# Performance work log

Measured on AMD Instinct MI355X. Metric: run time of the kernel, lower is better.

Reference implementation:

```python
import jax, jax.numpy as jnp
import numpy as np

INPUT_SIZE = 512
HIDDEN_SIZE = 512
BATCH = 64
SEQ = 1024

def _xavier(key, shape):
    fan_in, fan_out = shape
    limit = float(np.sqrt(6.0 / (fan_in + fan_out)))
    return jax.random.uniform(key, shape, jnp.float32, -limit, limit)

def setup_inputs() -> dict:
    key = jax.random.key(0)
    ks = jax.random.split(key, 9)
    x = jax.random.normal(ks[0], (BATCH, SEQ, INPUT_SIZE), jnp.float32)
    # Concatenate the 4 input-hidden and 4 hidden-hidden weights (i,f,g,o order)
    W_i = jnp.concatenate([_xavier(ks[1 + j], (INPUT_SIZE, HIDDEN_SIZE)) for j in range(4)], axis=1)  # [I, 4H]
    W_h = jnp.concatenate([_xavier(ks[5 + j], (HIDDEN_SIZE, HIDDEN_SIZE)) for j in range(4)], axis=1)  # [H, 4H]
    b = jnp.zeros((4 * HIDDEN_SIZE,), jnp.float32)  # b_ii+b_hi etc. are both zero-init; combined bias
    return {"x": x, "W_i": W_i, "W_h": W_h, "b": b}

def reference(x, W_i, W_h, b):
    H = W_h.shape[0]
    B = x.shape[0]
    # Precompute all input projections in one big GEMM: [B, S, 4H]
    x_proj = jnp.einsum('bsi,ig->bsg', x, W_i) + b

    def step(carry, xp_t):
        h, c = carry
        gates = xp_t + h @ W_h  # [B, 4H]
        i_t = jax.nn.sigmoid(gates[:, 0*H:1*H])
        f_t = jax.nn.sigmoid(gates[:, 1*H:2*H])
        g_t = jnp.tanh(gates[:, 2*H:3*H])
        o_t = jax.nn.sigmoid(gates[:, 3*H:4*H])
        c = f_t * c + i_t * g_t
        h = o_t * jnp.tanh(c)
        return (h, c), None

    h0 = jnp.zeros((B, H), x.dtype)
    c0 = jnp.zeros((B, H), x.dtype)
    (h_t, c_t), _ = jax.lax.scan(step, (h0, c0), jnp.swapaxes(x_proj, 0, 1))
    return (h_t, c_t)
```

## Files before the change

kernel.cpp:

```cpp
#include <hip/hip_runtime.h>
#include <hip/hip_bf16.h>
#include <hip/hip_cooperative_groups.h>

namespace cg = cooperative_groups;

typedef unsigned short ushort_t;
typedef unsigned int uint32;
typedef __attribute__((ext_vector_type(8))) __bf16 bf16x8;
typedef __attribute__((ext_vector_type(4))) float f32x4;
typedef __attribute__((ext_vector_type(4))) unsigned int u32x4;

#define SEQ_LEN 1024
#define NWG 32
#define NTHR 256

#define XPACK_BYTES (64ull << 20)
#define WPACK_BYTES (4ull << 20)
#define HB_OFF  (XPACK_BYTES + WPACK_BYTES)
#define FLG_OFF (HB_OFF + (128ull << 10))
#define WS_NEED (FLG_OFF + (4ull << 10))

__device__ __forceinline__ ushort_t f2bf(float f) {
  unsigned u = __builtin_bit_cast(unsigned, f);
  unsigned r = (u + 0x7fffu + ((u >> 16) & 1u)) >> 16;
  return (ushort_t)r;
}
__device__ __forceinline__ float sigm(float x) {
  float e = __expf(-x);
  return __builtin_amdgcn_rcpf(1.f + e);
}
__device__ __forceinline__ float tanh_fast(float x) {
  float a = fabsf(x);
  float e = __expf(-2.f * a);
  float r = (1.f - e) * __builtin_amdgcn_rcpf(1.f + e);
  return copysignf(r, x);
}

__global__ void zero_mem_kernel(u32x4* p) {
  int i = blockIdx.x * blockDim.x + threadIdx.x;
  u32x4 z = {0u, 0u, 0u, 0u};
  p[i] = z;
}

__global__ void pack_x_kernel(const float* __restrict__ x, u32x4* __restrict__ xp) {
  unsigned u = blockIdx.x * blockDim.x + threadIdx.x;
  int lane = u & 63;
  int kk   = (u >> 6) & 15;
  int bq   = (u >> 10) & 3;
  int t    = u >> 12;
  int hi2 = lane >> 4, lo = lane & 15;
  int b  = bq * 16 + lo;
  int k0 = kk * 32 + hi2 * 8;
  const float* src = x + ((size_t)b * SEQ_LEN + t) * 512 + k0;
  f32x4 f0 = *(const f32x4*)(src);
  f32x4 f1 = *(const f32x4*)(src + 4);
  u32x4 o;
  o[0] = f2bf(f0[0]) | ((uint32)f2bf(f0[1]) << 16);
  o[1] = f2bf(f0[2]) | ((uint32)f2bf(f0[3]) << 16);
  o[2] = f2bf(f1[0]) | ((uint32)f2bf(f1[1]) << 16);
  o[3] = f2bf(f1[2]) | ((uint32)f2bf(f1[3]) << 16);
  xp[u] = o;
}

__global__ void pack_w_kernel(const float* __restrict__ Wi, const float* __restrict__ Wh,
                              ushort_t* __restrict__ wp) {
  unsigned e = blockIdx.x * blockDim.x + threadIdx.x;
  int k = e >> 11;
  int col = e & 2047;
  float v = (k < 512) ? Wi[(size_t)k * 2048 + col] : Wh[(size_t)(k - 512) * 2048 + col];
  int wg  = (col & 511) >> 4;
  int tau = (col >> 2) & 3;
  int hcl = col & 3;
  int gate = col >> 9;
  int p = (hcl << 2) | gate;
  int kk = k >> 5;
  int hi = (k >> 3) & 3;
  int r = k & 7;
  int lane = (hi << 4) | p;
  wp[(size_t)wg * 65536 + (size_t)((kk * 4 + tau) * 64 + lane) * 8 + r] = f2bf(v);
}

template<bool FAST>
__global__ void __launch_bounds__(NTHR, 1)
lstm_coop(const float* __restrict__ x, const float* __restrict__ Wi,
          const float* __restrict__ Wh, const float* __restrict__ bias,
          const u32x4* __restrict__ xpack, const u32x4* __restrict__ wpack,
          ushort_t* hbuf, uint32* flags, float* out)
{
  __shared__ u32x4 lA[8192];
  const int tid  = threadIdx.x;
  const int wg   = blockIdx.x;
  const int lane = tid & 63;
  const int wv   = tid >> 6;
  const int hi2  = lane >> 4;
  const int lo   = lane & 15;
  const int b    = (wv << 4) | lo;

  if constexpr (FAST) {
    const u32x4* wsrc = wpack + (size_t)wg * 8192;
    for (int i = tid; i < 8192; i += NTHR) lA[i] = wsrc[i];
  } else {
    for (int uu = tid; uu < 8192; uu += NTHR) {
      int ln = uu & 63, tau = (uu >> 6) & 3, kk = uu >> 8;
      int uhi = ln >> 4, p = ln & 15;
      int gate = p & 3, hcl = p >> 2;
      int col = gate * 512 + (wg << 4) + tau * 4 + hcl;
      ushort_t tmp[8];
#pragma unroll
      for (int r = 0; r < 8; ++r) {
        int k = (kk << 5) + (uhi << 3) + r;
        float f = (k < 512) ? Wi[(size_t)k * 2048 + col] : Wh[(size_t)(k - 512) * 2048 + col];
        tmp[r] = f2bf(f);
      }
      u32x4 v;
      v[0] = tmp[0] | ((uint32)tmp[1] << 16);
      v[1] = tmp[2] | ((uint32)tmp[3] << 16);
      v[2] = tmp[4] | ((uint32)tmp[5] << 16);
      v[3] = tmp[6] | ((uint32)tmp[7] << 16);
      lA[uu] = v;
    }
  }
  __syncthreads();

  int kh[4], uoff[4];
  float bia[4][4];
#pragma unroll
  for (int tau = 0; tau < 4; ++tau) {
    int k = (wg << 4) + tau * 4 + hi2;
    kh[tau] = k;
    uoff[tau] = ((wv * 1024 + (k >> 5) * 64 + ((k >> 3) & 3) * 16 + lo) << 3) + (k & 7);
#pragma unroll
    for (int g = 0; g < 4; ++g) bia[tau][g] = bias[g * 512 + k];
  }

  float c[4] = {0.f, 0.f, 0.f, 0.f};
  float hn[4] = {0.f, 0.f, 0.f, 0.f};

  for (int t = 0; t < SEQ_LEN; ++t) {
    f32x4 ax0 = {bia[0][0], bia[0][1], bia[0][2], bia[0][3]};
    f32x4 ax1 = {bia[1][0], bia[1][1], bia[1][2], bia[1][3]};
    f32x4 ax2 = {bia[2][0], bia[2][1], bia[2][2], bia[2][3]};
    f32x4 ax3 = {bia[3][0], bia[3][1], bia[3][2], bia[3][3]};
#pragma unroll
    for (int kk = 0; kk < 16; ++kk) {
      bf16x8 xv;
      if constexpr (FAST) {
        xv = __builtin_bit_cast(bf16x8, xpack[(size_t)t * 4096 + wv * 1024 + kk * 64 + lane]);
      } else {
        const float* xr = x + ((size_t)b * SEQ_LEN + t) * 512 + (kk << 5) + (hi2 << 3);
        f32x4 f0 = *(const f32x4*)(xr);
        f32x4 f1 = *(const f32x4*)(xr + 4);
        u32x4 v;
        v[0] = f2bf(f0[0]) | ((uint32)f2bf(f0[1]) << 16);
        v[1] = f2bf(f0[2]) | ((uint32)f2bf(f0[3]) << 16);
        v[2] = f2bf(f1[0]) | ((uint32)f2bf(f1[1]) << 16);
        v[3] = f2bf(f1[2]) | ((uint32)f2bf(f1[3]) << 16);
        xv = __builtin_bit_cast(bf16x8, v);
      }
      ax0 = __builtin_amdgcn_mfma_f32_16x16x32_bf16(
              __builtin_bit_cast(bf16x8, lA[(kk * 4 + 0) * 64 + lane]), xv, ax0, 0, 0, 0);
      ax1 = __builtin_amdgcn_mfma_f32_16x16x32_bf16(
              __builtin_bit_cast(bf16x8, lA[(kk * 4 + 1) * 64 + lane]), xv, ax1, 0, 0, 0);
      ax2 = __builtin_amdgcn_mfma_f32_16x16x32_bf16(
              __builtin_bit_cast(bf16x8, lA[(kk * 4 + 2) * 64 + lane]), xv, ax2, 0, 0, 0);
      ax3 = __builtin_amdgcn_mfma_f32_16x16x32_bf16(
              __builtin_bit_cast(bf16x8, lA[(kk * 4 + 3) * 64 + lane]), xv, ax3, 0, 0, 0);
    }

    if (t > 0) {
      if constexpr (FAST) {
        const uint32* fa = flags + wv * 32 + (lane & 31);
        const uint32 tt = (uint32)t;
        while (true) {
          uint32 v;
          asm volatile("global_load_dword %0, %1, off sc0 sc1\n\ts_waitcnt vmcnt(0)"
                       : "=v"(v) : "v"(fa) : "memory");
          if (__all(v >= tt)) break;
        }
        __builtin_amdgcn_sched_barrier(0);
      }
      const u32x4* hr = (const u32x4*)(hbuf + (size_t)(t & 1) * 32768) + wv * 1024 + lane;
      u32x4 hreg[16];
      if constexpr (FAST) {
#pragma unroll
        for (int kk = 0; kk < 16; ++kk)
          asm volatile("global_load_dwordx4 %0, %1, off sc0 sc1"
                       : "=v"(hreg[kk]) : "v"(hr + kk * 64) : "memory");
        asm volatile("s_waitcnt vmcnt(0)" ::: "memory");
        __builtin_amdgcn_sched_barrier(0);
      } else {
#pragma unroll
        for (int kk = 0; kk < 16; ++kk) hreg[kk] = hr[kk * 64];
      }
#pragma unroll
      for (int kk = 0; kk < 16; ++kk) {
        bf16x8 hv = __builtin_bit_cast(bf16x8, hreg[kk]);
        ax0 = __builtin_amdgcn_mfma_f32_16x16x32_bf16(
                __builtin_bit_cast(bf16x8, lA[((16 + kk) * 4 + 0) * 64 + lane]), hv, ax0, 0, 0, 0);
        ax1 = __builtin_amdgcn_mfma_f32_16x16x32_bf16(
                __builtin_bit_cast(bf16x8, lA[((16 + kk) * 4 + 1) * 64 + lane]), hv, ax1, 0, 0, 0);
        ax2 = __builtin_amdgcn_mfma_f32_16x16x32_bf16(
                __builtin_bit_cast(bf16x8, lA[((16 + kk) * 4 + 2) * 64 + lane]), hv, ax2, 0, 0, 0);
        ax3 = __builtin_amdgcn_mfma_f32_16x16x32_bf16(
                __builtin_bit_cast(bf16x8, lA[((16 + kk) * 4 + 3) * 64 + lane]), hv, ax3, 0, 0, 0);
      }
    }

    f32x4 axv[4] = {ax0, ax1, ax2, ax3};
#pragma unroll
    for (int tau = 0; tau < 4; ++tau) {
      float gi = axv[tau][0], gf = axv[tau][1], gg = axv[tau][2], go = axv[tau][3];
      float it = sigm(gi), ft = sigm(gf), ot = sigm(go), gt = tanh_fast(gg);
      c[tau] = ft * c[tau] + it * gt;
      hn[tau] = ot * tanh_fast(c[tau]);
    }

    if (t < SEQ_LEN - 1) {
      ushort_t* hw = hbuf + (size_t)((t + 1) & 1) * 32768;
      if constexpr (FAST) {
#pragma unroll
        for (int tau = 0; tau < 4; ++tau) {
          uint32 v = f2bf(hn[tau]);
          asm volatile("global_store_short %0, %1, off sc0 sc1"
                       :: "v"(hw + uoff[tau]), "v"(v) : "memory");
        }
        asm volatile("s_waitcnt vmcnt(0)" ::: "memory");
        __builtin_amdgcn_sched_barrier(0);
        if (lane == 0) {
          uint32* fp = flags + wv * 32 + wg;
          uint32 val = (uint32)(t + 1);
          asm volatile("global_store_dword %0, %1, off sc0 sc1"
                       :: "v"(fp), "v"(val) : "memory");
        }
      } else {
#pragma unroll
        for (int tau = 0; tau < 4; ++tau) hw[uoff[tau]] = f2bf(hn[tau]);
        __threadfence();
        cg::this_grid().sync();
        __threadfence();
      }
    } else {
      if constexpr (!FAST) {
        __threadfence();
        cg::this_grid().sync();
      }
    }
  }

#pragma unroll
  for (int tau = 0; tau < 4; ++tau) {
    out[(size_t)b * 512 + kh[tau]] = hn[tau];
    out[32768 + (size_t)b * 512 + kh[tau]] = c[tau];
  }
}

extern "C" void kernel_launch(void* const* d_in, const int* in_sizes, int n_in,
                              void* d_out, int out_size, void* d_ws, size_t ws_size,
                              hipStream_t stream) {
  const float* x    = (const float*)d_in[0];
  const float* Wi   = (const float*)d_in[1];
  const float* Wh   = (const float*)d_in[2];
  const float* bias = (const float*)d_in[3];
  float* out = (float*)d_out;

  bool fast = (d_ws != nullptr) && (ws_size >= WS_NEED);

  if (fast) {
    const u32x4* xpack = (const u32x4*)d_ws;
    const u32x4* wpack = (const u32x4*)((char*)d_ws + XPACK_BYTES);
    ushort_t* hbuf = (ushort_t*)((char*)d_ws + HB_OFF);
    uint32* flags  = (uint32*)((char*)d_ws + FLG_OFF);

    zero_mem_kernel<<<1, 32, 0, stream>>>((u32x4*)((char*)d_ws + FLG_OFF));
    pack_x_kernel<<<16384, 256, 0, stream>>>(x, (u32x4*)d_ws);
    pack_w_kernel<<<8192, 256, 0, stream>>>(Wi, Wh, (ushort_t*)((char*)d_ws + XPACK_BYTES));

    lstm_coop<true><<<dim3(NWG), dim3(NTHR), 0, stream>>>(
        x, Wi, Wh, bias, xpack, wpack, hbuf, flags, out);
  } else {
    ushort_t* hbuf = (ushort_t*)d_out;
    uint32* flags = (uint32*)d_out;
    const u32x4* xpack = (const u32x4*)x;
    const u32x4* wpack = (const u32x4*)Wi;

    void* args[] = {(void*)&x, (void*)&Wi, (void*)&Wh, (void*)&bias,
                    (void*)&xpack, (void*)&wpack, (void*)&hbuf, (void*)&flags, (void*)&out};
    void (*kfn)(const float*, const float*, const float*, const float*,
                const u32x4*, const u32x4*, ushort_t*, uint32*, float*) = lstm_coop<false>;
    hipLaunchCooperativeKernel(reinterpret_cast<void*>(kfn), dim3(NWG), dim3(NTHR),
                               args, 0, stream);
  }
}
```

Measured before the change: 3.883 ms.

## Split LSTM into producer/consumer workgroups with ring-buffered input projections

Replaces the single persistent kernel with 64 workgroups of 512 threads. 32 producer workgroups compute the input projection x·W_i plus bias up to 16 timesteps ahead and write it into a flag-guarded ring buffer in the workspace. 32 consumer workgroups keep W_h in registers and run only the recurrent h·W_h matmul and gate math on the serial critical path. This removes the separate x-packing pass and takes the input GEMM off the per-step dependency chain. The cost is more flag polling, extra global traffic through the ring, and a reliance on all 64 workgroups being resident at once.

```diff
diff --git a/kernel.cpp b/kernel.cpp
--- a/kernel.cpp
+++ b/kernel.cpp
@@ -11,14 +11,14 @@
 typedef __attribute__((ext_vector_type(4))) unsigned int u32x4;
 
 #define SEQ_LEN 1024
-#define NWG 32
-#define NTHR 256
-
-#define XPACK_BYTES (64ull << 20)
-#define WPACK_BYTES (4ull << 20)
-#define HB_OFF  (XPACK_BYTES + WPACK_BYTES)
-#define FLG_OFF (HB_OFF + (128ull << 10))
-#define WS_NEED (FLG_OFF + (4ull << 10))
+#define RSLOT 16
+
+#define WPACK_OFF 0ull
+#define RING_OFF  (4ull << 20)
+#define HX_OFF    (RING_OFF + (8ull << 20))
+#define HFLG_OFF  (HX_OFF + (128ull << 10))
+#define XFLG_OFF  (HFLG_OFF + (1ull << 10))
+#define WS_NEED   (XFLG_OFF + (1ull << 10))
 
 __device__ __forceinline__ ushort_t f2bf(float f) {
   unsigned u = __builtin_bit_cast(unsigned, f);
@@ -35,31 +35,12 @@
   float r = (1.f - e) * __builtin_amdgcn_rcpf(1.f + e);
   return copysignf(r, x);
 }
+__device__ __forceinline__ uint32 umin2(uint32 a, uint32 b) { return a < b ? a : b; }
 
 __global__ void zero_mem_kernel(u32x4* p) {
   int i = blockIdx.x * blockDim.x + threadIdx.x;
   u32x4 z = {0u, 0u, 0u, 0u};
   p[i] = z;
-}
-
-__global__ void pack_x_kernel(const float* __restrict__ x, u32x4* __restrict__ xp) {
-  unsigned u = blockIdx.x * blockDim.x + threadIdx.x;
-  int lane = u & 63;
-  int kk   = (u >> 6) & 15;
-  int bq   = (u >> 10) & 3;
-  int t    = u >> 12;
-  int hi2 = lane >> 4, lo = lane & 15;
-  int b  = bq * 16 + lo;
-  int k0 = kk * 32 + hi2 * 8;
-  const float* src = x + ((size_t)b * SEQ_LEN + t) * 512 + k0;
-  f32x4 f0 = *(const f32x4*)(src);
-  f32x4 f1 = *(const f32x4*)(src + 4);
-  u32x4 o;
-  o[0] = f2bf(f0[0]) | ((uint32)f2bf(f0[1]) << 16);
-  o[1] = f2bf(f0[2]) | ((uint32)f2bf(f0[3]) << 16);
-  o[2] = f2bf(f1[0]) | ((uint32)f2bf(f1[1]) << 16);
-  o[3] = f2bf(f1[2]) | ((uint32)f2bf(f1[3]) << 16);
-  xp[u] = o;
 }
 
 __global__ void pack_w_kernel(const float* __restrict__ Wi, const float* __restrict__ Wh,
@@ -68,24 +49,227 @@
   int k = e >> 11;
   int col = e & 2047;
   float v = (k < 512) ? Wi[(size_t)k * 2048 + col] : Wh[(size_t)(k - 512) * 2048 + col];
-  int wg  = (col & 511) >> 4;
-  int tau = (col >> 2) & 3;
-  int hcl = col & 3;
+  int tile = (col & 511) >> 2;
+  int hcl  = col & 3;
   int gate = col >> 9;
   int p = (hcl << 2) | gate;
-  int kk = k >> 5;
+  int part = k >> 9;
+  int kk = (k >> 5) & 15;
   int hi = (k >> 3) & 3;
   int r = k & 7;
   int lane = (hi << 4) | p;
-  wp[(size_t)wg * 65536 + (size_t)((kk * 4 + tau) * 64 + lane) * 8 + r] = f2bf(v);
-}
-
-template<bool FAST>
-__global__ void __launch_bounds__(NTHR, 1)
-lstm_coop(const float* __restrict__ x, const float* __restrict__ Wi,
+  wp[(size_t)((tile * 32 + part * 16 + kk) * 64 + lane) * 8 + r] = f2bf(v);
+}
+
+__global__ __launch_bounds__(512, 1) void lstm_fast(
+    const float* __restrict__ x, const float* __restrict__ bias,
+    const u32x4* __restrict__ wpack, uint32* __restrict__ ring,
+    ushort_t* __restrict__ hx, uint32* __restrict__ hflg,
+    uint32* __restrict__ xflg, float* __restrict__ out)
+{
+  const int tid  = threadIdx.x;
+  const int lane = tid & 63;
+  const int wv   = tid >> 6;
+  const int bq   = wv & 3;
+  const int th   = wv >> 2;
+  const int hi2  = lane >> 4;
+  const int lo   = lane & 15;
+  const int b    = bq * 16 + lo;
+
+  const bool consumer = (blockIdx.x < 32);
+  const int wgr   = consumer ? blockIdx.x : (blockIdx.x - 32);
+  const int pair  = wgr * 2 + th;
+  const int tileA = pair * 2, tileB = pair * 2 + 1;
+  const int pid   = wgr * 8 + wv;
+  const int khA   = pair * 8 + hi2;
+  const int khB   = khA + 4;
+
+  if (consumer) {
+    bf16x8 wA[16], wB[16];
+    {
+      const u32x4* wa = wpack + ((size_t)tileA * 32 + 16) * 64 + lane;
+      const u32x4* wb = wpack + ((size_t)tileB * 32 + 16) * 64 + lane;
+#pragma unroll
+      for (int kk = 0; kk < 16; ++kk) {
+        wA[kk] = __builtin_bit_cast(bf16x8, wa[kk * 64]);
+        wB[kk] = __builtin_bit_cast(bf16x8, wb[kk * 64]);
+      }
+    }
+    const int hoffA = ((bq * 16 + (khA >> 5)) * 64 + ((khA >> 3) & 3) * 16 + lo) * 8 + (khA & 7);
+    const int hoffB = ((bq * 16 + (khB >> 5)) * 64 + ((khB >> 3) & 3) * 16 + lo) * 8 + (khB & 7);
+
+    float cA = 0.f, cB = 0.f, hA = 0.f, hB = 0.f;
+
+    for (int t = 0; t < SEQ_LEN; ++t) {
+      {
+        const uint32* xfp = xflg + pid;
+        const u32x4* hfp = (const u32x4*)hflg + lane;
+        const uint32 need_x = (uint32)(t + 1);
+        const uint32 need_h = (uint32)t;
+        while (true) {
+          uint32 xf; u32x4 hf;
+          asm volatile("global_load_dword %0, %2, off sc0 sc1\n\t"
+                       "global_load_dwordx4 %1, %3, off sc0 sc1\n\t"
+                       "s_waitcnt vmcnt(0)"
+                       : "=&v"(xf), "=&v"(hf) : "v"(xfp), "v"(hfp) : "memory");
+          __builtin_amdgcn_sched_barrier(0);
+          uint32 mn = umin2(umin2(hf[0], hf[1]), umin2(hf[2], hf[3]));
+          bool ok = (xf >= need_x) && (t == 0 || mn >= need_h);
+          if (__all(ok)) break;
+        }
+      }
+      u32x4 xpAu, xpBu;
+      {
+        const u32x4* rbase = (const u32x4*)ring + ((size_t)(t & (RSLOT - 1)) * 128) * 256;
+        const u32x4* rpA = rbase + ((size_t)tileA * 4 + bq) * 64 + lane;
+        const u32x4* rpB = rbase + ((size_t)tileB * 4 + bq) * 64 + lane;
+        asm volatile("global_load_dwordx4 %0, %1, off sc0 sc1"
+                     : "=v"(xpAu) : "v"(rpA) : "memory");
+        asm volatile("global_load_dwordx4 %0, %1, off sc0 sc1"
+                     : "=v"(xpBu) : "v"(rpB) : "memory");
+      }
+      f32x4 gA, gB;
+      if (t == 0) {
+        asm volatile("s_waitcnt vmcnt(0)" ::: "memory");
+        __builtin_amdgcn_sched_barrier(0);
+        gA = __builtin_bit_cast(f32x4, xpAu);
+        gB = __builtin_bit_cast(f32x4, xpBu);
+      } else {
+        u32x4 hreg[16];
+        const u32x4* hr = (const u32x4*)(hx + (size_t)(t & 1) * 32768) + bq * 1024 + lane;
+#pragma unroll
+        for (int kk = 0; kk < 16; ++kk)
+          asm volatile("global_load_dwordx4 %0, %1, off sc0 sc1"
+                       : "=v"(hreg[kk]) : "v"(hr + kk * 64) : "memory");
+        asm volatile("s_waitcnt vmcnt(0)" ::: "memory");
+        __builtin_amdgcn_sched_barrier(0);
+        f32x4 aA0 = __builtin_bit_cast(f32x4, xpAu);
+        f32x4 aB0 = __builtin_bit_cast(f32x4, xpBu);
+        f32x4 aA1 = {0.f, 0.f, 0.f, 0.f};
+        f32x4 aB1 = {0.f, 0.f, 0.f, 0.f};
+#pragma unroll
+        for (int kk = 0; kk < 16; kk += 2) {
+          bf16x8 h0 = __builtin_bit_cast(bf16x8, hreg[kk]);
+          bf16x8 h1 = __builtin_bit_cast(bf16x8, hreg[kk + 1]);
+          aA0 = __builtin_amdgcn_mfma_f32_16x16x32_bf16(wA[kk], h0, aA0, 0, 0, 0);
+          aB0 = __builtin_amdgcn_mfma_f32_16x16x32_bf16(wB[kk], h0, aB0, 0, 0, 0);
+          aA1 = __builtin_amdgcn_mfma_f32_16x16x32_bf16(wA[kk + 1], h1, aA1, 0, 0, 0);
+          aB1 = __builtin_amdgcn_mfma_f32_16x16x32_bf16(wB[kk + 1], h1, aB1, 0, 0, 0);
+        }
+        gA = aA0 + aA1;
+        gB = aB0 + aB1;
+      }
+      {
+        float it = sigm(gA[0]), ft = sigm(gA[1]), ot = sigm(gA[3]), gt = tanh_fast(gA[2]);
+        cA = ft * cA + it * gt;
+        hA = ot * tanh_fast(cA);
+      }
+      {
+        float it = sigm(gB[0]), ft = sigm(gB[1]), ot = sigm(gB[3]), gt = tanh_fast(gB[2]);
+        cB = ft * cB + it * gt;
+        hB = ot * tanh_fast(cB);
+      }
+      if (t < SEQ_LEN - 1) {
+        ushort_t* hw = hx + (size_t)((t + 1) & 1) * 32768;
+        uint32 vA = f2bf(hA), vB = f2bf(hB);
+        asm volatile("global_store_short %0, %1, off sc0 sc1"
+                     :: "v"(hw + hoffA), "v"(vA) : "memory");
+        asm volatile("global_store_short %0, %1, off sc0 sc1"
+                     :: "v"(hw + hoffB), "v"(vB) : "memory");
+        asm volatile("s_waitcnt vmcnt(0)" ::: "memory");
+        __builtin_amdgcn_sched_barrier(0);
+        if (lane == 0) {
+          uint32* fp = hflg + pid;
+          uint32 val = (uint32)(t + 1);
+          asm volatile("global_store_dword %0, %1, off sc0 sc1"
+                       :: "v"(fp), "v"(val) : "memory");
+        }
+      }
+    }
+    out[(size_t)b * 512 + khA] = hA;
+    out[(size_t)b * 512 + khB] = hB;
+    out[32768 + (size_t)b * 512 + khA] = cA;
+    out[32768 + (size_t)b * 512 + khB] = cB;
+  } else {
+    bf16x8 wA[16], wB[16];
+    {
+      const u32x4* wa = wpack + ((size_t)tileA * 32) * 64 + lane;
+      const u32x4* wb = wpack + ((size_t)tileB * 32) * 64 + lane;
+#pragma unroll
+      for (int kk = 0; kk < 16; ++kk) {
+        wA[kk] = __builtin_bit_cast(bf16x8, wa[kk * 64]);
+        wB[kk] = __builtin_bit_cast(bf16x8, wb[kk * 64]);
+      }
+    }
+    f32x4 biaA = {bias[0 * 512 + khA], bias[1 * 512 + khA],
+                  bias[2 * 512 + khA], bias[3 * 512 + khA]};
+    f32x4 biaB = {bias[0 * 512 + khB], bias[1 * 512 + khB],
+                  bias[2 * 512 + khB], bias[3 * 512 + khB]};
+
+    for (int t = 0; t < SEQ_LEN; ++t) {
+      bf16x8 xv[16];
+      {
+        const float* xr = x + ((size_t)b * SEQ_LEN + t) * 512 + (hi2 << 3);
+#pragma unroll
+        for (int kk = 0; kk < 16; ++kk) {
+          f32x4 f0 = *(const f32x4*)(xr + (kk << 5));
+          f32x4 f1 = *(const f32x4*)(xr + (kk << 5) + 4);
+          u32x4 v;
+          v[0] = f2bf(f0[0]) | ((uint32)f2bf(f0[1]) << 16);
+          v[1] = f2bf(f0[2]) | ((uint32)f2bf(f0[3]) << 16);
+          v[2] = f2bf(f1[0]) | ((uint32)f2bf(f1[1]) << 16);
+          v[3] = f2bf(f1[2]) | ((uint32)f2bf(f1[3]) << 16);
+          xv[kk] = __builtin_bit_cast(bf16x8, v);
+        }
+      }
+      if (t >= RSLOT) {
+        const uint32* gp = hflg + pid;
+        const uint32 need = (uint32)(t - RSLOT + 1);
+        while (true) {
+          uint32 v;
+          asm volatile("global_load_dword %0, %1, off sc0 sc1\n\ts_waitcnt vmcnt(0)"
+                       : "=v"(v) : "v"(gp) : "memory");
+          if (__all(v >= need)) break;
+        }
+        __builtin_amdgcn_sched_barrier(0);
+      }
+      f32x4 aA0 = biaA, aB0 = biaB;
+      f32x4 aA1 = {0.f, 0.f, 0.f, 0.f};
+      f32x4 aB1 = {0.f, 0.f, 0.f, 0.f};
+#pragma unroll
+      for (int kk = 0; kk < 16; kk += 2) {
+        aA0 = __builtin_amdgcn_mfma_f32_16x16x32_bf16(wA[kk], xv[kk], aA0, 0, 0, 0);
+        aB0 = __builtin_amdgcn_mfma_f32_16x16x32_bf16(wB[kk], xv[kk], aB0, 0, 0, 0);
+        aA1 = __builtin_amdgcn_mfma_f32_16x16x32_bf16(wA[kk + 1], xv[kk + 1], aA1, 0, 0, 0);
+        aB1 = __builtin_amdgcn_mfma_f32_16x16x32_bf16(wB[kk + 1], xv[kk + 1], aB1, 0, 0, 0);
+      }
+      u32x4 rA = __builtin_bit_cast(u32x4, aA0 + aA1);
+      u32x4 rB = __builtin_bit_cast(u32x4, aB0 + aB1);
+      {
+        u32x4* rbase = (u32x4*)ring + ((size_t)(t & (RSLOT - 1)) * 128) * 256;
+        u32x4* rpA = rbase + ((size_t)tileA * 4 + bq) * 64 + lane;
+        u32x4* rpB = rbase + ((size_t)tileB * 4 + bq) * 64 + lane;
+        asm volatile("global_store_dwordx4 %0, %1, off sc0 sc1"
+                     :: "v"(rpA), "v"(rA) : "memory");
+        asm volatile("global_store_dwordx4 %0, %1, off sc0 sc1"
+                     :: "v"(rpB), "v"(rB) : "memory");
+        asm volatile("s_waitcnt vmcnt(0)" ::: "memory");
+        __builtin_amdgcn_sched_barrier(0);
+        if (lane == 0) {
+          uint32* fp = xflg + pid;
+          uint32 val = (uint32)(t + 1);
+          asm volatile("global_store_dword %0, %1, off sc0 sc1"
+                       :: "v"(fp), "v"(val) : "memory");
+        }
+      }
+    }
+  }
+}
+
+__global__ void __launch_bounds__(256, 1)
+lstm_slow(const float* __restrict__ x, const float* __restrict__ Wi,
           const float* __restrict__ Wh, const float* __restrict__ bias,
-          const u32x4* __restrict__ xpack, const u32x4* __restrict__ wpack,
-          ushort_t* hbuf, uint32* flags, float* out)
+          ushort_t* hbuf, float* out)
 {
   __shared__ u32x4 lA[8192];
   const int tid  = threadIdx.x;
@@ -96,29 +280,24 @@
   const int lo   = lane & 15;
   const int b    = (wv << 4) | lo;
 
-  if constexpr (FAST) {
-    const u32x4* wsrc = wpack + (size_t)wg * 8192;
-    for (int i = tid; i < 8192; i += NTHR) lA[i] = wsrc[i];
-  } else {
-    for (int uu = tid; uu < 8192; uu += NTHR) {
-      int ln = uu & 63, tau = (uu >> 6) & 3, kk = uu >> 8;
-      int uhi = ln >> 4, p = ln & 15;
-      int gate = p & 3, hcl = p >> 2;
-      int col = gate * 512 + (wg << 4) + tau * 4 + hcl;
-      ushort_t tmp[8];
-#pragma unroll
-      for (int r = 0; r < 8; ++r) {
-        int k = (kk << 5) + (uhi << 3) + r;
-        float f = (k < 512) ? Wi[(size_t)k * 2048 + col] : Wh[(size_t)(k - 512) * 2048 + col];
-        tmp[r] = f2bf(f);
-      }
-      u32x4 v;
-      v[0] = tmp[0] | ((uint32)tmp[1] << 16);
-      v[1] = tmp[2] | ((uint32)tmp[3] << 16);
-      v[2] = tmp[4] | ((uint32)tmp[5] << 16);
-      v[3] = tmp[6] | ((uint32)tmp[7] << 16);
-      lA[uu] = v;
-    }
+  for (int uu = tid; uu < 8192; uu += 256) {
+    int ln = uu & 63, tau = (uu >> 6) & 3, kk = uu >> 8;
+    int uhi = ln >> 4, p = ln & 15;
+    int gate = p & 3, hcl = p >> 2;
+    int col = gate * 512 + (wg << 4) + tau * 4 + hcl;
+    ushort_t tmp[8];
+#pragma unroll
+    for (int r = 0; r < 8; ++r) {
+      int k = (kk << 5) + (uhi << 3) + r;
+      float f = (k < 512) ? Wi[(size_t)k * 2048 + col] : Wh[(size_t)(k - 512) * 2048 + col];
+      tmp[r] = f2bf(f);
+    }
+    u32x4 v;
+    v[0] = tmp[0] | ((uint32)tmp[1] << 16);
+    v[1] = tmp[2] | ((uint32)tmp[3] << 16);
+    v[2] = tmp[4] | ((uint32)tmp[5] << 16);
+    v[3] = tmp[6] | ((uint32)tmp[7] << 16);
+    lA[uu] = v;
   }
   __syncthreads();
 
@@ -143,20 +322,15 @@
     f32x4 ax3 = {bia[3][0], bia[3][1], bia[3][2], bia[3][3]};
 #pragma unroll
     for (int kk = 0; kk < 16; ++kk) {
-      bf16x8 xv;
-      if constexpr (FAST) {
-        xv = __builtin_bit_cast(bf16x8, xpack[(size_t)t * 4096 + wv * 1024 + kk * 64 + lane]);
-      } else {
-        const float* xr = x + ((size_t)b * SEQ_LEN + t) * 512 + (kk << 5) + (hi2 << 3);
-        f32x4 f0 = *(const f32x4*)(xr);
-        f32x4 f1 = *(const f32x4*)(xr + 4);
-        u32x4 v;
-        v[0] = f2bf(f0[0]) | ((uint32)f2bf(f0[1]) << 16);
-        v[1] = f2bf(f0[2]) | ((uint32)f2bf(f0[3]) << 16);
-        v[2] = f2bf(f1[0]) | ((uint32)f2bf(f1[1]) << 16);
-        v[3] = f2bf(f1[2]) | ((uint32)f2bf(f1[3]) << 16);
-        xv = __builtin_bit_cast(bf16x8, v);
-      }
+      const float* xr = x + ((size_t)b * SEQ_LEN + t) * 512 + (kk << 5) + (hi2 << 3);
+      f32x4 f0 = *(const f32x4*)(xr);
+      f32x4 f1 = *(const f32x4*)(xr + 4);
+      u32x4 v;
+      v[0] = f2bf(f0[0]) | ((uint32)f2bf(f0[1]) << 16);
+      v[1] = f2bf(f0[2]) | ((uint32)f2bf(f0[3]) << 16);
+      v[2] = f2bf(f1[0]) | ((uint32)f2bf(f1[1]) << 16);
+      v[3] = f2bf(f1[2]) | ((uint32)f2bf(f1[3]) << 16);
+      bf16x8 xv = __builtin_bit_cast(bf16x8, v);
       ax0 = __builtin_amdgcn_mfma_f32_16x16x32_bf16(
               __builtin_bit_cast(bf16x8, lA[(kk * 4 + 0) * 64 + lane]), xv, ax0, 0, 0, 0);
       ax1 = __builtin_amdgcn_mfma_f32_16x16x32_bf16(
@@ -168,30 +342,10 @@
     }
 
     if (t > 0) {
-      if constexpr (FAST) {
-        const uint32* fa = flags + wv * 32 + (lane & 31);
-        const uint32 tt = (uint32)t;
-        while (true) {
-          uint32 v;
-          asm volatile("global_load_dword %0, %1, off sc0 sc1\n\ts_waitcnt vmcnt(0)"
-                       : "=v"(v) : "v"(fa) : "memory");
-          if (__all(v >= tt)) break;
-        }
-        __builtin_amdgcn_sched_barrier(0);
-      }
       const u32x4* hr = (const u32x4*)(hbuf + (size_t)(t & 1) * 32768) + wv * 1024 + lane;
       u32x4 hreg[16];
-      if constexpr (FAST) {
-#pragma unroll
-        for (int kk = 0; kk < 16; ++kk)
-          asm volatile("global_load_dwordx4 %0, %1, off sc0 sc1"
-                       : "=v"(hreg[kk]) : "v"(hr + kk * 64) : "memory");
-        asm volatile("s_waitcnt vmcnt(0)" ::: "memory");
-        __builtin_amdgcn_sched_barrier(0);
-      } else {
-#pragma unroll
-        for (int kk = 0; kk < 16; ++kk) hreg[kk] = hr[kk * 64];
-      }
+#pragma unroll
+      for (int kk = 0; kk < 16; ++kk) hreg[kk] = hr[kk * 64];
 #pragma unroll
       for (int kk = 0; kk < 16; ++kk) {
         bf16x8 hv = __builtin_bit_cast(bf16x8, hreg[kk]);
@@ -217,33 +371,14 @@
 
     if (t < SEQ_LEN - 1) {
       ushort_t* hw = hbuf + (size_t)((t + 1) & 1) * 32768;
-      if constexpr (FAST) {
-#pragma unroll
-        for (int tau = 0; tau < 4; ++tau) {
-          uint32 v = f2bf(hn[tau]);
-          asm volatile("global_store_short %0, %1, off sc0 sc1"
-                       :: "v"(hw + uoff[tau]), "v"(v) : "memory");
-        }
-        asm volatile("s_waitcnt vmcnt(0)" ::: "memory");
-        __builtin_amdgcn_sched_barrier(0);
-        if (lane == 0) {
-          uint32* fp = flags + wv * 32 + wg;
-          uint32 val = (uint32)(t + 1);
-          asm volatile("global_store_dword %0, %1, off sc0 sc1"
-                       :: "v"(fp), "v"(val) : "memory");
-        }
-      } else {
-#pragma unroll
-        for (int tau = 0; tau < 4; ++tau) hw[uoff[tau]] = f2bf(hn[tau]);
-        __threadfence();
-        cg::this_grid().sync();
-        __threadfence();
-      }
+#pragma unroll
+      for (int tau = 0; tau < 4; ++tau) hw[uoff[tau]] = f2bf(hn[tau]);
+      __threadfence();
+      cg::this_grid().sync();
+      __threadfence();
     } else {
-      if constexpr (!FAST) {
-        __threadfence();
-        cg::this_grid().sync();
-      }
+      __threadfence();
+      cg::this_grid().sync();
     }
   }
 
@@ -266,28 +401,25 @@
   bool fast = (d_ws != nullptr) && (ws_size >= WS_NEED);
 
   if (fast) {
-    const u32x4* xpack = (const u32x4*)d_ws;
-    const u32x4* wpack = (const u32x4*)((char*)d_ws + XPACK_BYTES);
-    ushort_t* hbuf = (ushort_t*)((char*)d_ws + HB_OFF);
-    uint32* flags  = (uint32*)((char*)d_ws + FLG_OFF);
-
-    zero_mem_kernel<<<1, 32, 0, stream>>>((u32x4*)((char*)d_ws + FLG_OFF));
-    pack_x_kernel<<<16384, 256, 0, stream>>>(x, (u32x4*)d_ws);
-    pack_w_kernel<<<8192, 256, 0, stream>>>(Wi, Wh, (ushort_t*)((char*)d_ws + XPACK_BYTES));
-
-    lstm_coop<true><<<dim3(NWG), dim3(NTHR), 0, stream>>>(
-        x, Wi, Wh, bias, xpack, wpack, hbuf, flags, out);
+    const u32x4* wpack = (const u32x4*)((char*)d_ws + WPACK_OFF);
+    uint32* ring  = (uint32*)((char*)d_ws + RING_OFF);
+    ushort_t* hx  = (ushort_t*)((char*)d_ws + HX_OFF);
+    uint32* hflg  = (uint32*)((char*)d_ws + HFLG_OFF);
+    uint32* xflg  = (uint32*)((char*)d_ws + XFLG_OFF);
+
+    zero_mem_kernel<<<1, 128, 0, stream>>>((u32x4*)((char*)d_ws + HFLG_OFF));
+    pack_w_kernel<<<8192, 256, 0, stream>>>(Wi, Wh, (ushort_t*)((char*)d_ws + WPACK_OFF));
+
+    lstm_fast<<<dim3(64), dim3(512), 0, stream>>>(
+        x, bias, wpack, ring, hx, hflg, xflg, out);
   } else {
     ushort_t* hbuf = (ushort_t*)d_out;
-    uint32* flags = (uint32*)d_out;
-    const u32x4* xpack = (const u32x4*)x;
-    const u32x4* wpack = (const u32x4*)Wi;
 
     void* args[] = {(void*)&x, (void*)&Wi, (void*)&Wh, (void*)&bias,
-                    (void*)&xpack, (void*)&wpack, (void*)&hbuf, (void*)&flags, (void*)&out};
+                    (void*)&hbuf, (void*)&out};
     void (*kfn)(const float*, const float*, const float*, const float*,
-                const u32x4*, const u32x4*, ushort_t*, uint32*, float*) = lstm_coop<false>;
-    hipLaunchCooperativeKernel(reinterpret_cast<void*>(kfn), dim3(NWG), dim3(NTHR),
+                ushort_t*, float*) = lstm_slow;
+    hipLaunchCooperativeKernel(reinterpret_cast<void*>(kfn), dim3(32), dim3(256),
                                args, 0, stream);
   }
 }
```

After: 13.78 ms. 255% more time.

## Split LSTM into producer/recurrent warps, hold W_h in registers, widen grid

Applied to the files above, without the earlier changes.

The fast kernel now runs 64 workgroups of 512 threads. Four waves handle the serial recurrence while the other four compute the input projection for the next timestep into a double-buffered LDS slot, so the x@W_i work moves off the critical path. The recurrent W_h slice is kept in VGPRs instead of LDS, and the h@W_h MFMA chain is split into two accumulators to shorten the dependency. The risks are more workgroups polling flags each step, an extra __syncthreads per step, and heavy register pressure.

```diff
diff --git a/kernel.cpp b/kernel.cpp
--- a/kernel.cpp
+++ b/kernel.cpp
@@ -11,14 +11,12 @@
 typedef __attribute__((ext_vector_type(4))) unsigned int u32x4;
 
 #define SEQ_LEN 1024
-#define NWG 32
-#define NTHR 256
 
 #define XPACK_BYTES (64ull << 20)
-#define WPACK_BYTES (4ull << 20)
-#define HB_OFF  (XPACK_BYTES + WPACK_BYTES)
-#define FLG_OFF (HB_OFF + (128ull << 10))
-#define WS_NEED (FLG_OFF + (4ull << 10))
+#define WPACK_OFF   XPACK_BYTES
+#define HX_OFF      (WPACK_OFF + (4ull << 20))
+#define FLG_OFF     (HX_OFF + (128ull << 10))
+#define WS_NEED     (FLG_OFF + (4ull << 10))
 
 __device__ __forceinline__ ushort_t f2bf(float f) {
   unsigned u = __builtin_bit_cast(unsigned, f);
@@ -68,24 +66,184 @@
   int k = e >> 11;
   int col = e & 2047;
   float v = (k < 512) ? Wi[(size_t)k * 2048 + col] : Wh[(size_t)(k - 512) * 2048 + col];
-  int wg  = (col & 511) >> 4;
-  int tau = (col >> 2) & 3;
-  int hcl = col & 3;
+  int tile = (col & 511) >> 2;
+  int hcl  = col & 3;
   int gate = col >> 9;
   int p = (hcl << 2) | gate;
-  int kk = k >> 5;
+  int part = k >> 9;
+  int kk = (k >> 5) & 15;
   int hi = (k >> 3) & 3;
   int r = k & 7;
   int lane = (hi << 4) | p;
-  wp[(size_t)wg * 65536 + (size_t)((kk * 4 + tau) * 64 + lane) * 8 + r] = f2bf(v);
-}
-
-template<bool FAST>
-__global__ void __launch_bounds__(NTHR, 1)
-lstm_coop(const float* __restrict__ x, const float* __restrict__ Wi,
+  wp[(size_t)((tile * 32 + part * 16 + kk) * 64 + lane) * 8 + r] = f2bf(v);
+}
+
+__global__ __launch_bounds__(512, 1) void lstm_fast(
+    const u32x4* __restrict__ xpack, const u32x4* __restrict__ wpack,
+    const float* __restrict__ bias, ushort_t* __restrict__ hx,
+    uint32* __restrict__ flags, float* __restrict__ out)
+{
+  __shared__ u32x4 wiL[2048];
+  __shared__ f32x4 xbuf[2][2][4][64];
+
+  const int tid  = threadIdx.x;
+  const int wg   = blockIdx.x;
+  const int lane = tid & 63;
+  const int wv   = tid >> 6;
+  const bool rec = (wv < 4);
+  const int bq   = wv & 3;
+  const int hi2  = lane >> 4;
+  const int lo   = lane & 15;
+  const int b    = bq * 16 + lo;
+
+  for (int i = tid; i < 2048; i += 512) {
+    int ln = i & 63, tt = (i >> 6) & 1, kk = i >> 7;
+    wiL[i] = wpack[(size_t)(((2 * wg + tt) * 32 + kk) * 64) + ln];
+  }
+
+  bf16x8 wh0[16], wh1[16];
+  if (rec) {
+    const u32x4* wsA = wpack + (size_t)(((2 * wg + 0) * 32 + 16) * 64) + lane;
+    const u32x4* wsB = wpack + (size_t)(((2 * wg + 1) * 32 + 16) * 64) + lane;
+#pragma unroll
+    for (int kk = 0; kk < 16; ++kk) {
+      u32x4 a = wsA[kk * 64];
+      u32x4 c = wsB[kk * 64];
+      asm volatile("" : "+v"(a));
+      asm volatile("" : "+v"(c));
+      wh0[kk] = __builtin_bit_cast(bf16x8, a);
+      wh1[kk] = __builtin_bit_cast(bf16x8, c);
+    }
+  }
+  __syncthreads();
+
+  const int kh0 = wg * 8 + hi2;
+  const int kh1 = kh0 + 4;
+
+  f32x4 bia0, bia1;
+  if (!rec) {
+    bia0 = f32x4{bias[0 * 512 + kh0], bias[1 * 512 + kh0],
+                 bias[2 * 512 + kh0], bias[3 * 512 + kh0]};
+    bia1 = f32x4{bias[0 * 512 + kh1], bias[1 * 512 + kh1],
+                 bias[2 * 512 + kh1], bias[3 * 512 + kh1]};
+    f32x4 a0 = bia0, a1 = bia1;
+    const u32x4* xb = xpack + bq * 1024 + lane;
+#pragma unroll
+    for (int kk = 0; kk < 16; ++kk) {
+      bf16x8 xv = __builtin_bit_cast(bf16x8, xb[kk * 64]);
+      a0 = __builtin_amdgcn_mfma_f32_16x16x32_bf16(
+             __builtin_bit_cast(bf16x8, wiL[(kk * 2 + 0) * 64 + lane]), xv, a0, 0, 0, 0);
+      a1 = __builtin_amdgcn_mfma_f32_16x16x32_bf16(
+             __builtin_bit_cast(bf16x8, wiL[(kk * 2 + 1) * 64 + lane]), xv, a1, 0, 0, 0);
+    }
+    xbuf[0][0][bq][lane] = a0;
+    xbuf[0][1][bq][lane] = a1;
+  }
+
+  const int hoff0 = bq * 8192 + (((kh0 >> 5) * 64 + ((kh0 >> 3) & 3) * 16 + lo) << 3) + (kh0 & 7);
+  const int hoff1 = hoff0 + 4;
+
+  float c0 = 0.f, c1 = 0.f, h0v = 0.f, h1v = 0.f;
+
+  for (int t = 0; t < SEQ_LEN; ++t) {
+    __syncthreads();
+
+    if (rec) {
+      if (t > 0) {
+        const uint32* fp = flags + bq * 64 + lane;
+        const uint32 tt = (uint32)t;
+        while (true) {
+          uint32 v;
+          asm volatile("global_load_dword %0, %1, off sc0 sc1\n\ts_waitcnt vmcnt(0)"
+                       : "=v"(v) : "v"(fp) : "memory");
+          if (__all(v >= tt)) break;
+        }
+        __builtin_amdgcn_sched_barrier(0);
+      }
+      f32x4 g0 = xbuf[t & 1][0][bq][lane];
+      f32x4 g1 = xbuf[t & 1][1][bq][lane];
+
+      if (t > 0) {
+        const u32x4* hr = (const u32x4*)(hx + (size_t)(t & 1) * 32768) + bq * 1024 + lane;
+        u32x4 hreg[16];
+#pragma unroll
+        for (int kk = 0; kk < 16; ++kk)
+          asm volatile("global_load_dwordx4 %0, %1, off sc0 sc1"
+                       : "=v"(hreg[kk]) : "v"(hr + kk * 64) : "memory");
+        asm volatile("s_waitcnt vmcnt(0)" ::: "memory");
+        __builtin_amdgcn_sched_barrier(0);
+        f32x4 a00 = g0, a10 = g1;
+        f32x4 a01 = {0.f, 0.f, 0.f, 0.f};
+        f32x4 a11 = {0.f, 0.f, 0.f, 0.f};
+#pragma unroll
+        for (int kk = 0; kk < 16; kk += 2) {
+          bf16x8 hv0 = __builtin_bit_cast(bf16x8, hreg[kk]);
+          bf16x8 hv1 = __builtin_bit_cast(bf16x8, hreg[kk + 1]);
+          a00 = __builtin_amdgcn_mfma_f32_16x16x32_bf16(wh0[kk], hv0, a00, 0, 0, 0);
+          a10 = __builtin_amdgcn_mfma_f32_16x16x32_bf16(wh1[kk], hv0, a10, 0, 0, 0);
+          a01 = __builtin_amdgcn_mfma_f32_16x16x32_bf16(wh0[kk + 1], hv1, a01, 0, 0, 0);
+          a11 = __builtin_amdgcn_mfma_f32_16x16x32_bf16(wh1[kk + 1], hv1, a11, 0, 0, 0);
+        }
+        g0 = a00 + a01;
+        g1 = a10 + a11;
+      }
+      {
+        float it = sigm(g0[0]), ft = sigm(g0[1]), ot = sigm(g0[3]), gt = tanh_fast(g0[2]);
+        c0 = ft * c0 + it * gt;
+        h0v = ot * tanh_fast(c0);
+      }
+      {
+        float it = sigm(g1[0]), ft = sigm(g1[1]), ot = sigm(g1[3]), gt = tanh_fast(g1[2]);
+        c1 = ft * c1 + it * gt;
+        h1v = ot * tanh_fast(c1);
+      }
+      if (t < SEQ_LEN - 1) {
+        ushort_t* hw = hx + (size_t)((t + 1) & 1) * 32768;
+        uint32 v0 = f2bf(h0v), v1 = f2bf(h1v);
+        asm volatile("global_store_short %0, %1, off sc0 sc1"
+                     :: "v"(hw + hoff0), "v"(v0) : "memory");
+        asm volatile("global_store_short %0, %1, off sc0 sc1"
+                     :: "v"(hw + hoff1), "v"(v1) : "memory");
+        asm volatile("s_waitcnt vmcnt(0)" ::: "memory");
+        __builtin_amdgcn_sched_barrier(0);
+        if (lane == 0) {
+          uint32* fp = flags + bq * 64 + wg;
+          uint32 val = (uint32)(t + 1);
+          asm volatile("global_store_dword %0, %1, off sc0 sc1"
+                       :: "v"(fp), "v"(val) : "memory");
+        }
+      }
+    } else {
+      if (t + 1 < SEQ_LEN) {
+        const int tn = t + 1;
+        f32x4 a0 = bia0, a1 = bia1;
+        const u32x4* xb = xpack + (size_t)tn * 4096 + bq * 1024 + lane;
+#pragma unroll
+        for (int kk = 0; kk < 16; ++kk) {
+          bf16x8 xv = __builtin_bit_cast(bf16x8, xb[kk * 64]);
+          a0 = __builtin_amdgcn_mfma_f32_16x16x32_bf16(
+                 __builtin_bit_cast(bf16x8, wiL[(kk * 2 + 0) * 64 + lane]), xv, a0, 0, 0, 0);
+          a1 = __builtin_amdgcn_mfma_f32_16x16x32_bf16(
+                 __builtin_bit_cast(bf16x8, wiL[(kk * 2 + 1) * 64 + lane]), xv, a1, 0, 0, 0);
+        }
+        xbuf[tn & 1][0][bq][lane] = a0;
+        xbuf[tn & 1][1][bq][lane] = a1;
+      }
+    }
+  }
+
+  if (rec) {
+    out[(size_t)b * 512 + kh0] = h0v;
+    out[(size_t)b * 512 + kh1] = h1v;
+    out[32768 + (size_t)b * 512 + kh0] = c0;
+    out[32768 + (size_t)b * 512 + kh1] = c1;
+  }
+}
+
+__global__ void __launch_bounds__(256, 1)
+lstm_slow(const float* __restrict__ x, const float* __restrict__ Wi,
           const float* __restrict__ Wh, const float* __restrict__ bias,
-          const u32x4* __restrict__ xpack, const u32x4* __restrict__ wpack,
-          ushort_t* hbuf, uint32* flags, float* out)
+          ushort_t* hbuf, float* out)
 {
   __shared__ u32x4 lA[8192];
   const int tid  = threadIdx.x;
@@ -96,29 +254,24 @@
   const int lo   = lane & 15;
   const int b    = (wv << 4) | lo;
 
-  if constexpr (FAST) {
-    const u32x4* wsrc = wpack + (size_t)wg * 8192;
-    for (int i = tid; i < 8192; i += NTHR) lA[i] = wsrc[i];
-  } else {
-    for (int uu = tid; uu < 8192; uu += NTHR) {
-      int ln = uu & 63, tau = (uu >> 6) & 3, kk = uu >> 8;
-      int uhi = ln >> 4, p = ln & 15;
-      int gate = p & 3, hcl = p >> 2;
-      int col = gate * 512 + (wg << 4) + tau * 4 + hcl;
-      ushort_t tmp[8];
-#pragma unroll
-      for (int r = 0; r < 8; ++r) {
-        int k = (kk << 5) + (uhi << 3) + r;
-        float f = (k < 512) ? Wi[(size_t)k * 2048 + col] : Wh[(size_t)(k - 512) * 2048 + col];
-        tmp[r] = f2bf(f);
-      }
-      u32x4 v;
-      v[0] = tmp[0] | ((uint32)tmp[1] << 16);
-      v[1] = tmp[2] | ((uint32)tmp[3] << 16);
-      v[2] = tmp[4] | ((uint32)tmp[5] << 16);
-      v[3] = tmp[6] | ((uint32)tmp[7] << 16);
-      lA[uu] = v;
-    }
+  for (int uu = tid; uu < 8192; uu += 256) {
+    int ln = uu & 63, tau = (uu >> 6) & 3, kk = uu >> 8;
+    int uhi = ln >> 4, p = ln & 15;
+    int gate = p & 3, hcl = p >> 2;
+    int col = gate * 512 + (wg << 4) + tau * 4 + hcl;
+    ushort_t tmp[8];
+#pragma unroll
+    for (int r = 0; r < 8; ++r) {
+      int k = (kk << 5) + (uhi << 3) + r;
+      float f = (k < 512) ? Wi[(size_t)k * 2048 + col] : Wh[(size_t)(k - 512) * 2048 + col];
+      tmp[r] = f2bf(f);
+    }
+    u32x4 v;
+    v[0] = tmp[0] | ((uint32)tmp[1] << 16);
+    v[1] = tmp[2] | ((uint32)tmp[3] << 16);
+    v[2] = tmp[4] | ((uint32)tmp[5] << 16);
+    v[3] = tmp[6] | ((uint32)tmp[7] << 16);
+    lA[uu] = v;
   }
   __syncthreads();
 
@@ -143,20 +296,15 @@
     f32x4 ax3 = {bia[3][0], bia[3][1], bia[3][2], bia[3][3]};
 #pragma unroll
     for (int kk = 0; kk < 16; ++kk) {
-      bf16x8 xv;
-      if constexpr (FAST) {
-        xv = __builtin_bit_cast(bf16x8, xpack[(size_t)t * 4096 + wv * 1024 + kk * 64 + lane]);
-      } else {
-        const float* xr = x + ((size_t)b * SEQ_LEN + t) * 512 + (kk << 5) + (hi2 << 3);
-        f32x4 f0 = *(const f32x4*)(xr);
-        f32x4 f1 = *(const f32x4*)(xr + 4);
-        u32x4 v;
-        v[0] = f2bf(f0[0]) | ((uint32)f2bf(f0[1]) << 16);
-        v[1] = f2bf(f0[2]) | ((uint32)f2bf(f0[3]) << 16);
-        v[2] = f2bf(f1[0]) | ((uint32)f2bf(f1[1]) << 16);
-        v[3] = f2bf(f1[2]) | ((uint32)f2bf(f1[3]) << 16);
-        xv = __builtin_bit_cast(bf16x8, v);
-      }
+      const float* xr = x + ((size_t)b * SEQ_LEN + t) * 512 + (kk << 5) + (hi2 << 3);
+      f32x4 f0 = *(const f32x4*)(xr);
+      f32x4 f1 = *(const f32x4*)(xr + 4);
+      u32x4 v;
+      v[0] = f2bf(f0[0]) | ((uint32)f2bf(f0[1]) << 16);
+      v[1] = f2bf(f0[2]) | ((uint32)f2bf(f0[3]) << 16);
+      v[2] = f2bf(f1[0]) | ((uint32)f2bf(f1[1]) << 16);
+      v[3] = f2bf(f1[2]) | ((uint32)f2bf(f1[3]) << 16);
+      bf16x8 xv = __builtin_bit_cast(bf16x8, v);
       ax0 = __builtin_amdgcn_mfma_f32_16x16x32_bf16(
               __builtin_bit_cast(bf16x8, lA[(kk * 4 + 0) * 64 + lane]), xv, ax0, 0, 0, 0);
       ax1 = __builtin_amdgcn_mfma_f32_16x16x32_bf16(
@@ -168,30 +316,10 @@
     }
 
     if (t > 0) {
-      if constexpr (FAST) {
-        const uint32* fa = flags + wv * 32 + (lane & 31);
-        const uint32 tt = (uint32)t;
-        while (true) {
-          uint32 v;
-          asm volatile("global_load_dword %0, %1, off sc0 sc1\n\ts_waitcnt vmcnt(0)"
-                       : "=v"(v) : "v"(fa) : "memory");
-          if (__all(v >= tt)) break;
-        }
-        __builtin_amdgcn_sched_barrier(0);
-      }
       const u32x4* hr = (const u32x4*)(hbuf + (size_t)(t & 1) * 32768) + wv * 1024 + lane;
       u32x4 hreg[16];
-      if constexpr (FAST) {
-#pragma unroll
-        for (int kk = 0; kk < 16; ++kk)
-          asm volatile("global_load_dwordx4 %0, %1, off sc0 sc1"
-                       : "=v"(hreg[kk]) : "v"(hr + kk * 64) : "memory");
-        asm volatile("s_waitcnt vmcnt(0)" ::: "memory");
-        __builtin_amdgcn_sched_barrier(0);
-      } else {
-#pragma unroll
-        for (int kk = 0; kk < 16; ++kk) hreg[kk] = hr[kk * 64];
-      }
+#pragma unroll
+      for (int kk = 0; kk < 16; ++kk) hreg[kk] = hr[kk * 64];
 #pragma unroll
       for (int kk = 0; kk < 16; ++kk) {
         bf16x8 hv = __builtin_bit_cast(bf16x8, hreg[kk]);
@@ -215,36 +343,14 @@
       hn[tau] = ot * tanh_fast(c[tau]);
     }
 
+    ushort_t* hw = hbuf + (size_t)((t + 1) & 1) * 32768;
     if (t < SEQ_LEN - 1) {
-      ushort_t* hw = hbuf + (size_t)((t + 1) & 1) * 32768;
-      if constexpr (FAST) {
-#pragma unroll
-        for (int tau = 0; tau < 4; ++tau) {
-          uint32 v = f2bf(hn[tau]);
-          asm volatile("global_store_short %0, %1, off sc0 sc1"
-                       :: "v"(hw + uoff[tau]), "v"(v) : "memory");
-        }
-        asm volatile("s_waitcnt vmcnt(0)" ::: "memory");
-        __builtin_amdgcn_sched_barrier(0);
-        if (lane == 0) {
-          uint32* fp = flags + wv * 32 + wg;
-          uint32 val = (uint32)(t + 1);
-          asm volatile("global_store_dword %0, %1, off sc0 sc1"
-                       :: "v"(fp), "v"(val) : "memory");
-        }
-      } else {
-#pragma unroll
-        for (int tau = 0; tau < 4; ++tau) hw[uoff[tau]] = f2bf(hn[tau]);
-        __threadfence();
-        cg::this_grid().sync();
-        __threadfence();
-      }
-    } else {
-      if constexpr (!FAST) {
-        __threadfence();
-        cg::this_grid().sync();
-      }
-    }
+#pragma unroll
+      for (int tau = 0; tau < 4; ++tau) hw[uoff[tau]] = f2bf(hn[tau]);
+    }
+    __threadfence();
+    cg::this_grid().sync();
+    __threadfence();
   }
 
 #pragma unroll
@@ -267,27 +373,24 @@
 
   if (fast) {
     const u32x4* xpack = (const u32x4*)d_ws;
-    const u32x4* wpack = (const u32x4*)((char*)d_ws + XPACK_BYTES);
-    ushort_t* hbuf = (ushort_t*)((char*)d_ws + HB_OFF);
-    uint32* flags  = (uint32*)((char*)d_ws + FLG_OFF);
-
-    zero_mem_kernel<<<1, 32, 0, stream>>>((u32x4*)((char*)d_ws + FLG_OFF));
+    const u32x4* wpack = (const u32x4*)((char*)d_ws + WPACK_OFF);
+    ushort_t* hx  = (ushort_t*)((char*)d_ws + HX_OFF);
+    uint32* flags = (uint32*)((char*)d_ws + FLG_OFF);
+
+    zero_mem_kernel<<<1, 256, 0, stream>>>((u32x4*)((char*)d_ws + FLG_OFF));
     pack_x_kernel<<<16384, 256, 0, stream>>>(x, (u32x4*)d_ws);
-    pack_w_kernel<<<8192, 256, 0, stream>>>(Wi, Wh, (ushort_t*)((char*)d_ws + XPACK_BYTES));
-
-    lstm_coop<true><<<dim3(NWG), dim3(NTHR), 0, stream>>>(
-        x, Wi, Wh, bias, xpack, wpack, hbuf, flags, out);
+    pack_w_kernel<<<8192, 256, 0, stream>>>(Wi, Wh, (ushort_t*)((char*)d_ws + WPACK_OFF));
+
+    lstm_fast<<<dim3(64), dim3(512), 0, stream>>>(
+        xpack, wpack, bias, hx, flags, out);
   } else {
     ushort_t* hbuf = (ushort_t*)d_out;
-    uint32* flags = (uint32*)d_out;
-    const u32x4* xpack = (const u32x4*)x;
-    const u32x4* wpack = (const u32x4*)Wi;
 
     void* args[] = {(void*)&x, (void*)&Wi, (void*)&Wh, (void*)&bias,
-                    (void*)&xpack, (void*)&wpack, (void*)&hbuf, (void*)&flags, (void*)&out};
+                    (void*)&hbuf, (void*)&out};
     void (*kfn)(const float*, const float*, const float*, const float*,
-                const u32x4*, const u32x4*, ushort_t*, uint32*, float*) = lstm_coop<false>;
-    hipLaunchCooperativeKernel(reinterpret_cast<void*>(kfn), dim3(NWG), dim3(NTHR),
+                ushort_t*, float*) = lstm_slow;
+    hipLaunchCooperativeKernel(reinterpret_cast<void*>(kfn), dim3(32), dim3(256),
                                args, 0, stream);
   }
 }
```

Result: faster. 3.511 ms (-9.6%).
